# Kernel tuning notes

Measured on AMD Instinct MI355X. Metric: run time of the kernel, lower is better.

Reference implementation:

```python
import jax, jax.numpy as jnp
import numpy as np

NHEAD = 8
D_K = 64
BETA = 2.0
MIN_RBF = 0.01
MAX_RBF = 0.99
MIN_SPREAD, MAX_SPREAD, BASE, NUM_SPREAD = 1.0, 6.0, 20.0, 8
LN_EPS = 1e-5


def _spreads():
    # torch: min + (max-min) * (logspace(0,1,num,base) - 1) / (base - 1)
    return MIN_SPREAD + (MAX_SPREAD - MIN_SPREAD) * (BASE ** jnp.linspace(0.0, 1.0, NUM_SPREAD) - 1.0) / (BASE - 1.0)


def _layernorm(x, g, b):
    m = jnp.mean(x, axis=-1, keepdims=True)
    v = jnp.mean((x - m) ** 2, axis=-1, keepdims=True)
    return (x - m) * jax.lax.rsqrt(v + LN_EPS) * g + b


def setup_inputs() -> dict:
    key = jax.random.key(0)
    ks = jax.random.split(key, 12)
    B, N, D, H, K, DH = 4, 1024, 512, NHEAD, D_K, 1024
    s = 0.05
    return {
        "x": jax.random.normal(ks[0], (B, N, D), jnp.float32),
        "coords": jax.random.normal(ks[1], (B, N, 3), jnp.float32) * 8.0,  # Angstrom-scale spread
        "q_proj": jax.random.normal(ks[2], (H, D, K), jnp.float32) * s,
        "k_proj": jax.random.normal(ks[3], (H, D, K), jnp.float32) * s,
        "v_proj": jax.random.normal(ks[4], (H, D, K), jnp.float32) * s,
        "q_bias": jnp.zeros((H, K), jnp.float32),
        "k_bias": jnp.zeros((H, K), jnp.float32),
        "v_bias": jnp.zeros((H, K), jnp.float32),
        "w_out": jax.random.normal(ks[5], (D, D), jnp.float32) * s,
        "ln1_g": jnp.ones((D,), jnp.float32),
        "ln1_b": jnp.zeros((D,), jnp.float32),
        "w1": jax.random.normal(ks[6], (DH, D), jnp.float32) * s,
        "b1": jnp.zeros((DH,), jnp.float32),
        "w2": jax.random.normal(ks[7], (D, DH), jnp.float32) * s,
        "b2": jnp.zeros((D,), jnp.float32),
        "ln2_g": jnp.ones((D,), jnp.float32),
        "ln2_b": jnp.zeros((D,), jnp.float32),
    }


def reference(x, coords, q_proj, k_proj, v_proj, q_bias, k_bias, v_bias,
              w_out, ln1_g, ln1_b, w1, b1, w2, b2, ln2_g, ln2_b):
    B, N, D = x.shape
    # per-head QKV projections: [B,H,N,K]
    Q = jnp.einsum('bnd,hdk->bhnk', x, q_proj) + q_bias[None, :, None, :]
    K_ = jnp.einsum('bnd,hdk->bhnk', x, k_proj) + k_bias[None, :, None, :]
    V = jnp.einsum('bnd,hdk->bhnk', x, v_proj) + v_bias[None, :, None, :]

    S = jnp.einsum('bhnk,bhmk->bhnm', Q, K_) / np.float32(np.sqrt(D_K))

    # pairwise squared distances [B,N,N] and per-head gaussian RBFs [B,H,N,N]
    d2 = jnp.sum((coords[:, :, None, :] - coords[:, None, :, :]) ** 2, axis=-1)
    spreads = _spreads().astype(x.dtype)  # [H]
    rbf = jnp.exp(-d2[:, None, :, :] / (2.0 * spreads[None, :, None, None] ** 2))
    valid = (rbf >= MIN_RBF) & (rbf <= MAX_RBF)  # sparse attention band

    # probs proportional to exp(S) * rbf**beta, restricted to the valid band
    logits = jnp.where(valid, S + BETA * jnp.log(jnp.maximum(rbf, 1e-12)), -1e9)
    p = jax.nn.softmax(logits, axis=-1)
    p = jnp.where(valid, p, 0.0)  # fully-masked rows -> zero output

    o = jnp.einsum('bhnm,bhmk->bhnk', p, V)
    # torch: out.permute(0,2,3,1).reshape(B,N,D) -> interleave (d_k, head)
    o = o.transpose(0, 2, 3, 1).reshape(B, N, D)
    attn_out = o @ w_out.T

    x = _layernorm(x + attn_out, ln1_g, ln1_b)
    h = jax.nn.gelu(x @ w1.T + b1)
    ffn = h @ w2.T + b2
    x = _layernorm(x + ffn, ln2_g, ln2_b)
    return x
```

## Files before the change

### kernel.cpp

```cpp
#include <hip/hip_runtime.h>
#include <cmath>

typedef short s16x8 __attribute__((ext_vector_type(8)));
typedef float f32x4 __attribute__((ext_vector_type(4)));
typedef unsigned short u16;

#define MFMA(a, b, c) __builtin_amdgcn_mfma_f32_16x16x32_bf16((a), (b), (c), 0, 0, 0)

__device__ inline u16 f2b(float f) {
    union { float f; unsigned u; } v; v.f = f;
    unsigned r = v.u + 0x7fffu + ((v.u >> 16) & 1u);
    return (u16)(r >> 16);
}

__device__ inline void glds16(const u16* g, u16* l) {
    __builtin_amdgcn_global_load_lds(
        (const __attribute__((address_space(1))) unsigned int*)g,
        (__attribute__((address_space(3))) unsigned int*)l, 16, 0, 0);
}

__global__ __launch_bounds__(256) void prep_kernel(
    const float* __restrict__ x,
    const float* __restrict__ qp, const float* __restrict__ kp, const float* __restrict__ vp,
    const float* __restrict__ w_out, const float* __restrict__ w1, const float* __restrict__ w2,
    u16* __restrict__ xb, u16* __restrict__ Bqkv, u16* __restrict__ w_outp,
    u16* __restrict__ w1b, u16* __restrict__ w2b)
{
    const int NXV = 262144;
    const int NQKV = 786432;
    const int NWO = 262144;
    const int NW1 = 524288;
    const int NW2 = 524288;
    const int TOT = NXV + NQKV + NWO + NW1 + NW2;
    for (int i = blockIdx.x * 256 + threadIdx.x; i < TOT; i += gridDim.x * 256) {
        int j = i;
        if (j < NXV) {
            const int base = j * 8;
            float4 a0 = *(const float4*)(x + base);
            float4 a1 = *(const float4*)(x + base + 4);
            s16x8 o;
            o[0]=f2b(a0.x); o[1]=f2b(a0.y); o[2]=f2b(a0.z); o[3]=f2b(a0.w);
            o[4]=f2b(a1.x); o[5]=f2b(a1.y); o[6]=f2b(a1.z); o[7]=f2b(a1.w);
            *(s16x8*)(xb + base) = o;
            continue;
        }
        j -= NXV;
        if (j < NQKV) {
            const int k = j & 63, d = (j >> 6) & 511, zh = j >> 15;
            const int z = zh >> 3, h = zh & 7;
            const float* W = (z == 0) ? qp : (z == 1) ? kp : vp;
            const float v = W[h * 32768 + d * 64 + k];
            Bqkv[(z * 512 + h * 64 + k) * 512 + d] = f2b(v);
            continue;
        }
        j -= NQKV;
        if (j < NWO) {
            const int oc = j & 511, row = j >> 9;
            const int h = oc >> 6, k = oc & 63;
            w_outp[j] = f2b(w_out[row * 512 + k * 8 + h]);
            continue;
        }
        j -= NWO;
        if (j < NW1) { w1b[j] = f2b(w1[j]); continue; }
        j -= NW1;
        w2b[j] = f2b(w2[j]);
    }
}

template<int TM>
__device__ inline void gemm_core(const u16* __restrict__ A, const u16* __restrict__ B,
                                 int K, int ktiles, int kstart, int r0, int c0,
                                 u16* As, u16* Bs, f32x4 (&acc)[TM / 32][4])
{
    const int t = threadIdx.x, lane = t & 63, wid = t >> 6;
    const int l15 = lane & 15, lg = lane >> 4, sw = l15 & 7;
    constexpr int FR = TM / 32;
    const int wr = (wid & 1) * (TM / 2), wc = (wid >> 1) * 64;
    constexpr int NA = TM * 8 / 256;

    const f32x4 zero = {0.f, 0.f, 0.f, 0.f};
    #pragma unroll
    for (int fr = 0; fr < FR; ++fr)
        #pragma unroll
        for (int fc = 0; fc < 4; ++fc) acc[fr][fc] = zero;

    for (int kt = 0; kt < ktiles; ++kt) {
        const int k0 = kstart + kt * 64;
        __syncthreads();
        #pragma unroll
        for (int i = 0; i < NA; ++i) {
            const int slot = i * 256 + t;
            const int row = slot >> 3, c = slot & 7;
            glds16(A + (size_t)(r0 + row) * K + k0 + ((c ^ (row & 7)) << 3),
                   As + i * 2048 + wid * 512);
        }
        #pragma unroll
        for (int i = 0; i < 4; ++i) {
            const int slot = i * 256 + t;
            const int row = slot >> 3, c = slot & 7;
            glds16(B + (size_t)(c0 + row) * K + k0 + ((c ^ (row & 7)) << 3),
                   Bs + i * 2048 + wid * 512);
        }
        __syncthreads();
        #pragma unroll
        for (int ks = 0; ks < 2; ++ks) {
            const int cc = ((ks * 4 + lg) ^ sw) * 8;
            s16x8 af[FR], bf[4];
            #pragma unroll
            for (int f = 0; f < FR; ++f)
                af[f] = *(const s16x8*)(As + (wr + f * 16 + l15) * 64 + cc);
            #pragma unroll
            for (int f = 0; f < 4; ++f)
                bf[f] = *(const s16x8*)(Bs + (wc + f * 16 + l15) * 64 + cc);
            #pragma unroll
            for (int fr = 0; fr < FR; ++fr)
                #pragma unroll
                for (int fc = 0; fc < 4; ++fc)
                    acc[fr][fc] = MFMA(af[fr], bf[fc], acc[fr][fc]);
        }
    }
}

#define SCALE_Q 0.18033688f
__global__ __launch_bounds__(256) void gemm_qkv_kernel(
    const u16* __restrict__ xb, const u16* __restrict__ Bqkv,
    const float* __restrict__ qb, const float* __restrict__ kb, const float* __restrict__ vb,
    u16* __restrict__ Qb, u16* __restrict__ Kb, u16* __restrict__ Vtb)
{
    __shared__ __align__(16) u16 As[64 * 64];
    __shared__ __align__(16) u16 Bs[128 * 64];
    f32x4 acc[2][4];
    const int r0 = blockIdx.x * 64, c0 = blockIdx.y * 128;
    gemm_core<64>(xb, Bqkv, 512, 8, 0, r0, c0, As, Bs, acc);

    const int t = threadIdx.x, lane = t & 63, wid = t >> 6;
    const int wr = (wid & 1) * 32, wc = (wid >> 1) * 64;
    const int l15 = lane & 15, lg = lane >> 4;

    #pragma unroll
    for (int fc = 0; fc < 4; ++fc) {
        const int gc = c0 + wc + fc * 16 + l15;
        const int z = gc >> 9;
        const int hk = gc & 511;
        const int h = hk >> 6, k = gc & 63;
        const float bias = (z == 0 ? qb : z == 1 ? kb : vb)[hk];
        #pragma unroll
        for (int fr = 0; fr < 2; ++fr) {
            #pragma unroll
            for (int r = 0; r < 4; ++r) {
                const int grow = r0 + wr + fr * 16 + lg * 4 + r;
                const int b = grow >> 10, n = grow & 1023;
                const int bh = b * 8 + h;
                float v = acc[fr][fc][r] + bias;
                if (z == 0) v *= SCALE_Q;
                const u16 val = f2b(v);
                if (z == 0)      Qb[(size_t)bh * 65536 + n * 64 + k] = val;
                else if (z == 1) Kb[(size_t)bh * 65536 + n * 64 + k] = val;
                else             Vtb[(size_t)bh * 65536 + k * 1024 + n] = val;
            }
        }
    }
}

template<int EPI>
__global__ __launch_bounds__(256) void gemm_kernel(
    const u16* __restrict__ A, const u16* __restrict__ B, const float* __restrict__ bias,
    float* __restrict__ Cf, u16* __restrict__ Cb, int N, int K, int ktiles, size_t pstride)
{
    __shared__ __align__(16) u16 As[64 * 64];
    __shared__ __align__(16) u16 Bs[128 * 64];
    f32x4 acc[2][4];
    const int r0 = blockIdx.x * 64, c0 = blockIdx.y * 128;
    const int kstart = blockIdx.z * ktiles * 64;
    gemm_core<64>(A, B, K, ktiles, kstart, r0, c0, As, Bs, acc);
    float* Cfz = Cf + (size_t)blockIdx.z * pstride;

    const int t = threadIdx.x, lane = t & 63, wid = t >> 6;
    const int wr = (wid & 1) * 32, wc = (wid >> 1) * 64;
    const int l15 = lane & 15, lg = lane >> 4;

    #pragma unroll
    for (int fc = 0; fc < 4; ++fc) {
        const int gc = c0 + wc + fc * 16 + l15;
        const float bv = (EPI == 2) ? bias[gc] : 0.f;
        #pragma unroll
        for (int fr = 0; fr < 2; ++fr) {
            #pragma unroll
            for (int r = 0; r < 4; ++r) {
                const int grow = r0 + wr + fr * 16 + lg * 4 + r;
                float v = acc[fr][fc][r] + bv;
                if (EPI == 2) {
                    const float u = 0.7978845608028654f * (v + 0.044715f * v * v * v);
                    v = 0.5f * v * (1.0f + tanhf(u));
                    Cb[(size_t)grow * N + gc] = f2b(v);
                } else {
                    Cfz[(size_t)grow * N + gc] = v;
                }
            }
        }
    }
}

struct AttnParams { float g2[8], lo[8], hi[8]; };

__global__ __launch_bounds__(512, 4) void attn_kernel(
    const u16* __restrict__ Qb, const u16* __restrict__ Kb, const u16* __restrict__ Vtb,
    const float* __restrict__ coords, float* __restrict__ Po, float* __restrict__ Lo,
    AttnParams prm)
{
    __shared__ __align__(16) u16 Ks[64 * 64];
    __shared__ __align__(16) u16 Vs[64 * 64];
    __shared__ __align__(16) u16 Ps[8][16][72];
    __shared__ float cmx[512], cmy[512], cmz[512];

    const int wg = blockIdx.x;
    const int swz = (wg & 7) * 64 + (wg >> 3);
    const int bh = swz >> 4;
    const int rest = swz & 15;
    const int n0 = (rest >> 1) * 128;
    const int z = rest & 1;
    const int b = bh >> 3, h = bh & 7;
    const float g2 = prm.g2[h], lo = prm.lo[h], hi = prm.hi[h];

    const int t = threadIdx.x, lane = t & 63, wid = t >> 6;
    const int l15 = lane & 15, lg = lane >> 4, sw = l15 & 7;
    const int wq0 = wid * 16;

    const u16* Kz = Kb + (size_t)bh * 65536 + (size_t)z * 32768;
    const u16* Vz = Vtb + (size_t)bh * 65536 + z * 512;

    {
        const float* c = coords + ((size_t)b * 1024 + z * 512 + t) * 3;
        cmx[t] = c[0]; cmy[t] = c[1]; cmz[t] = c[2];
    }

    s16x8 qf[2];
    {
        const u16* qp_ = Qb + (size_t)bh * 65536 + (size_t)(n0 + wq0 + l15) * 64;
        qf[0] = *(const s16x8*)(qp_ + lg * 8);
        qf[1] = *(const s16x8*)(qp_ + 32 + lg * 8);
    }
    float qx[4], qy[4], qz_[4];
    #pragma unroll
    for (int r = 0; r < 4; ++r) {
        const float* c = coords + ((size_t)b * 1024 + n0 + wq0 + lg * 4 + r) * 3;
        qx[r] = c[0]; qy[r] = c[1]; qz_[r] = c[2];
    }

    f32x4 o_acc[4];
    const f32x4 zero = {0.f, 0.f, 0.f, 0.f};
    float l_lane[4] = {0.f, 0.f, 0.f, 0.f};
    #pragma unroll
    for (int kf = 0; kf < 4; ++kf) o_acc[kf] = zero;

    for (int mt = 0; mt < 8; ++mt) {
        {
            const int row = t >> 3, c = t & 7;
            const int cc = (c ^ (row & 7)) << 3;
            glds16(Kz + (size_t)(mt * 64 + row) * 64 + cc, Ks + wid * 512);
            glds16(Vz + (size_t)row * 1024 + mt * 64 + cc, Vs + wid * 512);
        }
        __syncthreads();

        float mx[4], my[4], mz[4];
        #pragma unroll
        for (int mf = 0; mf < 4; ++mf) {
            const int mloc = mt * 64 + mf * 16 + l15;
            mx[mf] = cmx[mloc]; my[mf] = cmy[mloc]; mz[mf] = cmz[mloc];
        }

        f32x4 s[4];
        #pragma unroll
        for (int mf = 0; mf < 4; ++mf) {
            const int row = mf * 16 + l15;
            s16x8 kf0 = *(const s16x8*)(Ks + row * 64 + ((lg ^ sw) << 3));
            s16x8 kf1 = *(const s16x8*)(Ks + row * 64 + (((4 + lg) ^ sw) << 3));
            f32x4 a = zero;
            a = MFMA(qf[0], kf0, a);
            a = MFMA(qf[1], kf1, a);
            s[mf] = a;
        }

        s16x8 vfr[2][4];
        #pragma unroll
        for (int ms = 0; ms < 2; ++ms)
            #pragma unroll
            for (int kf = 0; kf < 4; ++kf) {
                const int row = kf * 16 + l15;
                vfr[ms][kf] = *(const s16x8*)(Vs + row * 64
                                              + (((ms * 4 + lg) ^ sw) << 3));
            }

        #pragma unroll
        for (int mf = 0; mf < 4; ++mf) {
            #pragma unroll
            for (int r = 0; r < 4; ++r) {
                const float dx = qx[r] - mx[mf], dy = qy[r] - my[mf], dz = qz_[r] - mz[mf];
                const float d2 = fmaf(dx, dx, fmaf(dy, dy, dz * dz));
                const bool valid = (d2 >= lo) && (d2 <= hi);
                float pv = exp2f(fmaf(d2, g2, s[mf][r]) - 8.0f);
                pv = valid ? pv : 0.f;
                l_lane[r] += pv;
                Ps[wid][lg * 4 + r][mf * 16 + l15] = f2b(pv);
            }
        }

        #pragma unroll
        for (int ms = 0; ms < 2; ++ms) {
            s16x8 pa = *(const s16x8*)&Ps[wid][l15][ms * 32 + lg * 8];
            #pragma unroll
            for (int kf = 0; kf < 4; ++kf)
                o_acc[kf] = MFMA(pa, vfr[ms][kf], o_acc[kf]);
        }

        __syncthreads();
    }

    #pragma unroll
    for (int r = 0; r < 4; ++r) {
        float v = l_lane[r];
        v += __shfl_xor(v, 1); v += __shfl_xor(v, 2);
        v += __shfl_xor(v, 4); v += __shfl_xor(v, 8);
        l_lane[r] = v;
    }

    float* PoZ = Po + (size_t)(z * 32 + bh) * 65536;
    #pragma unroll
    for (int kf = 0; kf < 4; ++kf)
        #pragma unroll
        for (int r = 0; r < 4; ++r) {
            const int n = n0 + wq0 + lg * 4 + r;
            PoZ[(size_t)n * 64 + kf * 16 + l15] = o_acc[kf][r];
        }
    if (l15 == 0) {
        #pragma unroll
        for (int r = 0; r < 4; ++r)
            Lo[z * 32768 + bh * 1024 + n0 + wq0 + lg * 4 + r] = l_lane[r];
    }
}

__global__ __launch_bounds__(256) void attn_merge_kernel(
    const float* __restrict__ Po, const float* __restrict__ Lo, u16* __restrict__ Ob)
{
    const int gid = blockIdx.x * 256 + threadIdx.x;
    const int row = gid >> 3;
    const int k0 = (gid & 7) * 8;
    const int bh = row >> 10, n = row & 1023;
    const int b = bh >> 3, h = bh & 7;
    const float l0 = Lo[row], l1 = Lo[32768 + row];
    const float lt = l0 + l1;
    const float invl = (lt > 0.f) ? 1.f / lt : 0.f;
    const float* p0 = Po + (size_t)row * 64 + k0;
    const float* p1 = Po + 2097152 + (size_t)row * 64 + k0;
    float4 a0 = *(const float4*)p0;
    float4 a1 = *(const float4*)(p0 + 4);
    float4 b0 = *(const float4*)p1;
    float4 b1 = *(const float4*)(p1 + 4);
    s16x8 o;
    o[0] = f2b((a0.x + b0.x) * invl);
    o[1] = f2b((a0.y + b0.y) * invl);
    o[2] = f2b((a0.z + b0.z) * invl);
    o[3] = f2b((a0.w + b0.w) * invl);
    o[4] = f2b((a1.x + b1.x) * invl);
    o[5] = f2b((a1.y + b1.y) * invl);
    o[6] = f2b((a1.z + b1.z) * invl);
    o[7] = f2b((a1.w + b1.w) * invl);
    *(s16x8*)(Ob + ((size_t)b * 1024 + n) * 512 + h * 64 + k0) = o;
}

template<bool CB, bool WB16>
__global__ __launch_bounds__(256) void add_ln_kernel(
    const float* __restrict__ a, const float* __restrict__ b0, const float* __restrict__ b1,
    const float* __restrict__ cb, const float* __restrict__ g, const float* __restrict__ bt,
    float* __restrict__ out, u16* __restrict__ outb)
{
    const int lane = threadIdx.x & 63;
    const int row = blockIdx.x * 4 + (threadIdx.x >> 6);
    const size_t base = (size_t)row * 512 + lane * 8;

    float v[8];
    {
        float4 a0 = *(const float4*)(a + base);
        float4 a1 = *(const float4*)(a + base + 4);
        float4 p0 = *(const float4*)(b0 + base);
        float4 p1 = *(const float4*)(b0 + base + 4);
        v[0]=a0.x+p0.x; v[1]=a0.y+p0.y; v[2]=a0.z+p0.z; v[3]=a0.w+p0.w;
        v[4]=a1.x+p1.x; v[5]=a1.y+p1.y; v[6]=a1.z+p1.z; v[7]=a1.w+p1.w;
        float4 q0 = *(const float4*)(b1 + base);
        float4 q1 = *(const float4*)(b1 + base + 4);
        v[0]+=q0.x; v[1]+=q0.y; v[2]+=q0.z; v[3]+=q0.w;
        v[4]+=q1.x; v[5]+=q1.y; v[6]+=q1.z; v[7]+=q1.w;
        if (CB) {
            float4 c0 = *(const float4*)(cb + lane * 8);
            float4 c1 = *(const float4*)(cb + lane * 8 + 4);
            v[0]+=c0.x; v[1]+=c0.y; v[2]+=c0.z; v[3]+=c0.w;
            v[4]+=c1.x; v[5]+=c1.y; v[6]+=c1.z; v[7]+=c1.w;
        }
    }
    float s = 0.f;
    #pragma unroll
    for (int k = 0; k < 8; ++k) s += v[k];
    #pragma unroll
    for (int m = 1; m <= 32; m <<= 1) s += __shfl_xor(s, m);
    const float mean = s * (1.0f / 512.0f);

    float vs = 0.f;
    #pragma unroll
    for (int k = 0; k < 8; ++k) { const float d = v[k] - mean; vs += d * d; }
    #pragma unroll
    for (int m = 1; m <= 32; m <<= 1) vs += __shfl_xor(vs, m);
    const float rstd = rsqrtf(vs * (1.0f / 512.0f) + 1e-5f);

    float4 g0 = *(const float4*)(g + lane * 8);
    float4 g1 = *(const float4*)(g + lane * 8 + 4);
    float4 t0 = *(const float4*)(bt + lane * 8);
    float4 t1 = *(const float4*)(bt + lane * 8 + 4);
    float gg[8] = {g0.x,g0.y,g0.z,g0.w,g1.x,g1.y,g1.z,g1.w};
    float tb[8] = {t0.x,t0.y,t0.z,t0.w,t1.x,t1.y,t1.z,t1.w};

    float o[8];
    #pragma unroll
    for (int k = 0; k < 8; ++k) o[k] = (v[k] - mean) * rstd * gg[k] + tb[k];
    float4 w0; w0.x=o[0]; w0.y=o[1]; w0.z=o[2]; w0.w=o[3];
    float4 w1; w1.x=o[4]; w1.y=o[5]; w1.z=o[6]; w1.w=o[7];
    *(float4*)(out + base) = w0;
    *(float4*)(out + base + 4) = w1;
    if (WB16) {
        s16x8 q;
        #pragma unroll
        for (int k = 0; k < 8; ++k) q[k] = (short)f2b(o[k]);
        *(s16x8*)(outb + base) = q;
    }
}

extern "C" void kernel_launch(void* const* d_in, const int* in_sizes, int n_in,
                              void* d_out, int out_size, void* d_ws, size_t ws_size,
                              hipStream_t stream)
{
    const float* x      = (const float*)d_in[0];
    const float* coords = (const float*)d_in[1];
    const float* qp     = (const float*)d_in[2];
    const float* kp     = (const float*)d_in[3];
    const float* vp     = (const float*)d_in[4];
    const float* qbias  = (const float*)d_in[5];
    const float* kbias  = (const float*)d_in[6];
    const float* vbias  = (const float*)d_in[7];
    const float* w_out  = (const float*)d_in[8];
    const float* ln1g   = (const float*)d_in[9];
    const float* ln1b   = (const float*)d_in[10];
    const float* w1     = (const float*)d_in[11];
    const float* b1     = (const float*)d_in[12];
    const float* w2     = (const float*)d_in[13];
    const float* b2     = (const float*)d_in[14];
    const float* ln2g   = (const float*)d_in[15];
    const float* ln2b   = (const float*)d_in[16];
    float* out = (float*)d_out;

    char* W = (char*)d_ws;
    u16*  xb     = (u16*)(W + 0);
    u16*  Bqkv   = (u16*)(W + 4194304);
    u16*  w_outp = (u16*)(W + 5767168);
    u16*  w1b    = (u16*)(W + 6291456);
    u16*  w2b    = (u16*)(W + 7340032);
    u16*  Qb     = (u16*)(W + 8388608);
    u16*  Kb     = (u16*)(W + 12582912);
    u16*  Vtb    = (u16*)(W + 16777216);
    u16*  Ob     = (u16*)(W + 20971520);
    float* X1    = (float*)(W + 25165824);
    u16*  Hb     = (u16*)(W + 33554432);
    float* P0    = (float*)(W + 41943040);
    float* P1    = P0 + 2097152;
    u16*  X1b    = Qb;
    float* Po    = P0;
    float* Lo    = X1;

    AttnParams prm;
    for (int h = 0; h < 8; ++h) {
        const double sg = 1.0 + 5.0 * (pow(20.0, (double)h / 7.0) - 1.0) / 19.0;
        const double s2 = sg * sg;
        prm.g2[h] = (float)(-1.4426950408889634 / s2);
        prm.lo[h] = (float)(2.0 * s2 * log(100.0 / 99.0));
        prm.hi[h] = (float)(2.0 * s2 * log(100.0));
    }

    prep_kernel<<<1024, 256, 0, stream>>>(x, qp, kp, vp, w_out, w1, w2,
                                          xb, Bqkv, w_outp, w1b, w2b);
    gemm_qkv_kernel<<<dim3(64, 12), 256, 0, stream>>>(xb, Bqkv, qbias, kbias, vbias,
                                                      Qb, Kb, Vtb);
    attn_kernel<<<512, 512, 0, stream>>>(Qb, Kb, Vtb, coords, Po, Lo, prm);
    attn_merge_kernel<<<1024, 256, 0, stream>>>(Po, Lo, Ob);
    gemm_kernel<0><<<dim3(64, 4, 2), 256, 0, stream>>>(Ob, w_outp, nullptr, P0, nullptr,
                                                       512, 512, 4, 2097152);
    add_ln_kernel<false, true><<<1024, 256, 0, stream>>>(x, P0, P1, nullptr,
                                                         ln1g, ln1b, X1, X1b);
    gemm_kernel<2><<<dim3(64, 8), 256, 0, stream>>>(X1b, w1b, b1, nullptr, Hb,
                                                    1024, 512, 8, 0);
    gemm_kernel<0><<<dim3(64, 4, 2), 256, 0, stream>>>(Hb, w2b, nullptr, P0, nullptr,
                                                       512, 1024, 8, 2097152);
    add_ln_kernel<true, false><<<1024, 256, 0, stream>>>(X1, P0, P1, b2,
                                                         ln2g, ln2b, out, nullptr);
}
```

Baseline: 119.6 us.

## Split attention key dimension four ways instead of two to double grid size

The attention kernel now splits the 1024 keys into four 256-key chunks per query tile instead of two, launching 1024 workgroups instead of 512. This gives the GPU more workgroups to fill its compute units. The merge kernel now sums four partial outputs and denominators, which adds extra partial-buffer traffic. The partial buffers are moved to larger workspace regions, overlapping xb and X1, which are free at that point.

```diff
diff --git a/kernel.cpp b/kernel.cpp
--- a/kernel.cpp
+++ b/kernel.cpp
@@ -211,14 +211,14 @@
     __shared__ __align__(16) u16 Ks[64 * 64];
     __shared__ __align__(16) u16 Vs[64 * 64];
     __shared__ __align__(16) u16 Ps[8][16][72];
-    __shared__ float cmx[512], cmy[512], cmz[512];
+    __shared__ float cmx[256], cmy[256], cmz[256];
 
     const int wg = blockIdx.x;
-    const int swz = (wg & 7) * 64 + (wg >> 3);
-    const int bh = swz >> 4;
-    const int rest = swz & 15;
-    const int n0 = (rest >> 1) * 128;
-    const int z = rest & 1;
+    const int swz = (wg & 7) * 128 + (wg >> 3);
+    const int bh = swz >> 5;
+    const int rest = swz & 31;
+    const int n0 = (rest >> 2) * 128;
+    const int z = rest & 3;
     const int b = bh >> 3, h = bh & 7;
     const float g2 = prm.g2[h], lo = prm.lo[h], hi = prm.hi[h];
 
@@ -226,11 +226,11 @@
     const int l15 = lane & 15, lg = lane >> 4, sw = l15 & 7;
     const int wq0 = wid * 16;
 
-    const u16* Kz = Kb + (size_t)bh * 65536 + (size_t)z * 32768;
-    const u16* Vz = Vtb + (size_t)bh * 65536 + z * 512;
-
-    {
-        const float* c = coords + ((size_t)b * 1024 + z * 512 + t) * 3;
+    const u16* Kz = Kb + (size_t)bh * 65536 + (size_t)z * 16384;
+    const u16* Vz = Vtb + (size_t)bh * 65536 + z * 256;
+
+    if (t < 256) {
+        const float* c = coords + ((size_t)b * 1024 + z * 256 + t) * 3;
         cmx[t] = c[0]; cmy[t] = c[1]; cmz[t] = c[2];
     }
 
@@ -253,7 +253,7 @@
     #pragma unroll
     for (int kf = 0; kf < 4; ++kf) o_acc[kf] = zero;
 
-    for (int mt = 0; mt < 8; ++mt) {
+    for (int mt = 0; mt < 4; ++mt) {
         {
             const int row = t >> 3, c = t & 7;
             const int cc = (c ^ (row & 7)) << 3;
@@ -347,24 +347,22 @@
     const int k0 = (gid & 7) * 8;
     const int bh = row >> 10, n = row & 1023;
     const int b = bh >> 3, h = bh & 7;
-    const float l0 = Lo[row], l1 = Lo[32768 + row];
-    const float lt = l0 + l1;
+    float lt = 0.f;
+    #pragma unroll
+    for (int zz = 0; zz < 4; ++zz) lt += Lo[zz * 32768 + row];
     const float invl = (lt > 0.f) ? 1.f / lt : 0.f;
-    const float* p0 = Po + (size_t)row * 64 + k0;
-    const float* p1 = Po + 2097152 + (size_t)row * 64 + k0;
-    float4 a0 = *(const float4*)p0;
-    float4 a1 = *(const float4*)(p0 + 4);
-    float4 b0 = *(const float4*)p1;
-    float4 b1 = *(const float4*)(p1 + 4);
+    float acc[8] = {0.f, 0.f, 0.f, 0.f, 0.f, 0.f, 0.f, 0.f};
+    #pragma unroll
+    for (int zz = 0; zz < 4; ++zz) {
+        const float* p = Po + (size_t)zz * 2097152 + (size_t)row * 64 + k0;
+        float4 a0 = *(const float4*)p;
+        float4 a1 = *(const float4*)(p + 4);
+        acc[0] += a0.x; acc[1] += a0.y; acc[2] += a0.z; acc[3] += a0.w;
+        acc[4] += a1.x; acc[5] += a1.y; acc[6] += a1.z; acc[7] += a1.w;
+    }
     s16x8 o;
-    o[0] = f2b((a0.x + b0.x) * invl);
-    o[1] = f2b((a0.y + b0.y) * invl);
-    o[2] = f2b((a0.z + b0.z) * invl);
-    o[3] = f2b((a0.w + b0.w) * invl);
-    o[4] = f2b((a1.x + b1.x) * invl);
-    o[5] = f2b((a1.y + b1.y) * invl);
-    o[6] = f2b((a1.z + b1.z) * invl);
-    o[7] = f2b((a1.w + b1.w) * invl);
+    #pragma unroll
+    for (int i = 0; i < 8; ++i) o[i] = f2b(acc[i] * invl);
     *(s16x8*)(Ob + ((size_t)b * 1024 + n) * 512 + h * 64 + k0) = o;
 }
 
@@ -471,8 +469,8 @@
     float* P0    = (float*)(W + 41943040);
     float* P1    = P0 + 2097152;
     u16*  X1b    = Qb;
-    float* Po    = P0;
-    float* Lo    = X1;
+    float* Po    = (float*)(W + 25165824);
+    float* Lo    = (float*)(W + 0);
 
     AttnParams prm;
     for (int h = 0; h < 8; ++h) {
@@ -487,7 +485,7 @@
                                           xb, Bqkv, w_outp, w1b, w2b);
     gemm_qkv_kernel<<<dim3(64, 12), 256, 0, stream>>>(xb, Bqkv, qbias, kbias, vbias,
                                                       Qb, Kb, Vtb);
-    attn_kernel<<<512, 512, 0, stream>>>(Qb, Kb, Vtb, coords, Po, Lo, prm);
+    attn_kernel<<<1024, 512, 0, stream>>>(Qb, Kb, Vtb, coords, Po, Lo, prm);
     attn_merge_kernel<<<1024, 256, 0, stream>>>(Po, Lo, Ob);
     gemm_kernel<0><<<dim3(64, 4, 2), 256, 0, stream>>>(Ob, w_outp, nullptr, P0, nullptr,
                                                        512, 512, 4, 2097152);
```

After: 123.7 us. 3.4% more time.
